# Kernel optimization log

Measured on AMD Instinct MI355X. Metric: run time of the kernel, lower is better.

Reference implementation:

```python
import jax, jax.numpy as jnp
import numpy as np

N_NODES = 50000
N_EDGES = 800000
IN_C, HID_C, OUT_C = 256, 256, 128


def setup_inputs() -> dict:
    key = jax.random.key(0)
    k1, k2, k3, k4 = jax.random.split(key, 4)
    x = jax.random.normal(k1, (N_NODES, IN_C), dtype=jnp.float32)
    edge_index = jax.random.randint(k2, (2, N_EDGES), 0, N_NODES, dtype=jnp.int64)
    W1 = jax.random.normal(k3, (IN_C, HID_C), dtype=jnp.float32) / np.sqrt(IN_C)
    b1 = jnp.zeros((HID_C,), dtype=jnp.float32)
    W2 = jax.random.normal(k4, (HID_C, OUT_C), dtype=jnp.float32) / np.sqrt(HID_C)
    b2 = jnp.zeros((OUT_C,), dtype=jnp.float32)
    return {"x": x, "edge_index": edge_index, "W1": W1, "b1": b1, "W2": W2, "b2": b2}


def _gcn_norm(edge_index, n_nodes):
    # Add self-loops, compute symmetric normalization D^-1/2 (A+I) D^-1/2 (PyG GCNConv default).
    loop = jnp.arange(n_nodes, dtype=edge_index.dtype)
    src = jnp.concatenate([edge_index[0], loop])  # [E+N]
    dst = jnp.concatenate([edge_index[1], loop])  # [E+N]
    deg = jax.ops.segment_sum(jnp.ones_like(dst, dtype=jnp.float32), dst, num_segments=n_nodes)
    dinv = jnp.where(deg > 0, 1.0 / jnp.sqrt(deg), 0.0)
    norm = dinv[src] * dinv[dst]  # [E+N]
    return src, dst, norm


def _gcn_conv(x, src, dst, norm, W, b, n_nodes):
    h = x @ W                                  # [N, out] dense GEMM first (PyG order)
    msg = h[src] * norm[:, None]               # gather + scale: [E+N, out]
    out = jax.ops.segment_sum(msg, dst, num_segments=n_nodes)  # scatter-add
    return out + b


def reference(x, edge_index, W1, b1, W2, b2):
    n = x.shape[0]
    src, dst, norm = _gcn_norm(edge_index, n)
    h = _gcn_conv(x, src, dst, norm, W1, b1, n)
    h = jax.nn.relu(h)
    # dropout is identity in eval mode
    return _gcn_conv(h, src, dst, norm, W2, b2, n)
```

## Files before the change

kernel.cpp:

```cpp
#include <hip/hip_runtime.h>
#include <cstdint>
#include <cstddef>


static constexpr int CH1 = 256;
static constexpr int CH2 = 128;

typedef __attribute__((ext_vector_type(8))) short bf16x8;
typedef __attribute__((ext_vector_type(4))) float f32x4;
typedef __attribute__((ext_vector_type(4))) unsigned short u16x4;

__device__ inline unsigned short f2bf(float f) {
  unsigned u = __builtin_bit_cast(unsigned, f);
  return (unsigned short)((u + 0x7fffu + ((u >> 16) & 1u)) >> 16);
}
__device__ inline float bf2f(unsigned short h) {
  return __builtin_bit_cast(float, (unsigned)h << 16);
}
__device__ inline float lo16(unsigned u) { return __builtin_bit_cast(float, u << 16); }
__device__ inline float hi16(unsigned u) { return __builtin_bit_cast(float, u & 0xffff0000u); }

__device__ inline void gload16(const void* g, void* l) {
  __builtin_amdgcn_global_load_lds(
      (const __attribute__((address_space(1))) unsigned int*)g,
      (__attribute__((address_space(3))) unsigned int*)l, 16, 0, 0);
}


__global__ void k_set_int(int* p, int v) { *p = v; }

__global__ void k_zero_int(int* __restrict__ p, int n) {
  int i = blockIdx.x * blockDim.x + threadIdx.x;
  if (i < n) p[i] = 0;
}

__global__ void k_detect_i32(const unsigned int* __restrict__ w, int nwords,
                             int* __restrict__ flag) {
  int i = blockIdx.x * blockDim.x + threadIdx.x;
  if (i < nwords && (i & 1) && w[i] != 0u) *flag = 1;
}

__global__ void k_cvt_deg(const void* __restrict__ raw, int* __restrict__ e32,
                          int* __restrict__ deg, int E, const int* __restrict__ flag) {
  int i = blockIdx.x * blockDim.x + threadIdx.x;
  if (i >= 2 * E) return;
  int v = (*flag) ? ((const int*)raw)[i] : (int)((const long long*)raw)[i];
  e32[i] = v;
  if (i >= E) atomicAdd(&deg[v], 1);
}

__global__ __launch_bounds__(256) void k_chunk_sum(const int* __restrict__ deg,
                                                   int* __restrict__ bsum, int N) {
  __shared__ int sh[256];
  int i = blockIdx.x * 256 + threadIdx.x;
  sh[threadIdx.x] = (i < N) ? deg[i] : 0;
  __syncthreads();
  for (int off = 128; off > 0; off >>= 1) {
    if (threadIdx.x < (unsigned)off) sh[threadIdx.x] += sh[threadIdx.x + off];
    __syncthreads();
  }
  if (threadIdx.x == 0) bsum[blockIdx.x] = sh[0];
}

__global__ __launch_bounds__(256) void k_scan_bsums(int* __restrict__ bsum, int nb) {
  __shared__ int sh[256];
  int t = threadIdx.x;
  int v = (t < nb) ? bsum[t] : 0;
  sh[t] = v;
  __syncthreads();
  for (int off = 1; off < 256; off <<= 1) {
    int add = (t >= off) ? sh[t - off] : 0;
    __syncthreads();
    sh[t] += add;
    __syncthreads();
  }
  if (t < nb) bsum[t] = sh[t] - v;
}

__global__ __launch_bounds__(256) void k_chunk_scan(
    const int* __restrict__ deg, const int* __restrict__ bsum,
    int* __restrict__ rowstart, int* __restrict__ cursor,
    float* __restrict__ dinv, int N, int E) {
  __shared__ int sh[256];
  int t = threadIdx.x;
  int i = blockIdx.x * 256 + t;
  int d = (i < N) ? deg[i] : 0;
  sh[t] = d;
  __syncthreads();
  for (int off = 1; off < 256; off <<= 1) {
    int add = (t >= off) ? sh[t - off] : 0;
    __syncthreads();
    sh[t] += add;
    __syncthreads();
  }
  if (i < N) {
    int rs = bsum[blockIdx.x] + sh[t] - d;
    rowstart[i] = rs;
    cursor[i]   = rs;
    dinv[i] = rsqrtf((float)(d + 1));
  }
  if (i == 0) rowstart[N] = E;
}

__global__ void k_fill(const int* __restrict__ src, const int* __restrict__ dst,
                       int* __restrict__ cursor, int* __restrict__ csr, int E) {
  int e = blockIdx.x * blockDim.x + threadIdx.x;
  if (e < E) {
    int pos = atomicAdd(&cursor[dst[e]], 1);
    csr[pos] = src[e];
  }
}


__global__ void k_split4(const float4* __restrict__ in, u16x4* __restrict__ oh,
                         u16x4* __restrict__ ol, int n4) {
  int i = blockIdx.x * blockDim.x + threadIdx.x;
  if (i >= n4) return;
  float4 v = in[i];
  u16x4 h, l;
  h.x = f2bf(v.x); l.x = f2bf(v.x - bf2f(h.x));
  h.y = f2bf(v.y); l.y = f2bf(v.y - bf2f(h.y));
  h.z = f2bf(v.z); l.z = f2bf(v.z - bf2f(h.z));
  h.w = f2bf(v.w); l.w = f2bf(v.w - bf2f(h.w));
  oh[i] = h; ol[i] = l;
}

__global__ void k_splitT(const float* __restrict__ W, unsigned short* __restrict__ oh,
                         unsigned short* __restrict__ ol, int K, int N) {
  int idx = blockIdx.x * blockDim.x + threadIdx.x;
  if (idx >= K * N) return;
  int k = idx / N, n = idx - k * N;
  float v = W[idx];
  unsigned short h = f2bf(v);
  oh[(size_t)n * K + k] = h;
  ol[(size_t)n * K + k] = f2bf(v - bf2f(h));
}

template <int BN>
__global__ __launch_bounds__(256) void k_gemm_mfma(
    const unsigned short* __restrict__ Ah, const unsigned short* __restrict__ Al,
    const unsigned short* __restrict__ Bh, const unsigned short* __restrict__ Bl,
    unsigned short* __restrict__ Co, int M, int K) {
  constexpr int BM = 64, BK = 32;
  constexpr int NF = BN / 64;
  constexpr int ASZ = BM * BK;
  constexpr int BSZ = BN * BK;
  __shared__ unsigned short lds[2][2 * ASZ + 2 * BSZ];
  const int t = threadIdx.x;
  const int w = t >> 6, l = t & 63;
  const int m0 = blockIdx.x * BM;
  const int lr = l & 15, lk = l >> 4;

  auto stage = [&](int buf, int k0) {
    unsigned short* base = lds[buf];
    {
      int row = t >> 2, p = t & 3;
      int s = p ^ ((row >> 1) & 3);
      int gm = m0 + row; if (gm >= M) gm = M - 1;
      size_t go = (size_t)gm * K + k0 + s * 8;
      gload16(Ah + go, base + (size_t)row * BK + p * 8);
      gload16(Al + go, base + ASZ + (size_t)row * BK + p * 8);
    }
    for (int i = t; i < BN * 4; i += 256) {
      int n = i >> 2, p = i & 3;
      int s = p ^ ((n >> 1) & 3);
      size_t go = (size_t)n * K + k0 + s * 8;
      gload16(Bh + go, base + 2 * ASZ + (size_t)n * BK + p * 8);
      gload16(Bl + go, base + 2 * ASZ + BSZ + (size_t)n * BK + p * 8);
    }
  };

  f32x4 acc[4][NF];
#pragma unroll
  for (int a = 0; a < 4; ++a)
#pragma unroll
    for (int b = 0; b < NF; ++b) acc[a][b] = (f32x4){0.f, 0.f, 0.f, 0.f};

  stage(0, 0);
  __syncthreads();
  const int nsteps = K / BK;
  for (int ks = 0; ks < nsteps; ++ks) {
    int cur = ks & 1;
    if (ks + 1 < nsteps) stage(cur ^ 1, (ks + 1) * BK);
    const unsigned short* base = lds[cur];
    bf16x8 ah[4], al[4], bh[NF], bl[NF];
#pragma unroll
    for (int fm = 0; fm < 4; ++fm) {
      int row = fm * 16 + lr;
      int p = lk ^ ((row >> 1) & 3);
      const unsigned short* a = base + row * BK + p * 8;
      ah[fm] = *(const bf16x8*)a;
      al[fm] = *(const bf16x8*)(a + ASZ);
    }
#pragma unroll
    for (int fb = 0; fb < NF; ++fb) {
      int n = w * (BN / 4) + fb * 16 + lr;
      int p = lk ^ ((n >> 1) & 3);
      const unsigned short* b = base + 2 * ASZ + n * BK + p * 8;
      bh[fb] = *(const bf16x8*)b;
      bl[fb] = *(const bf16x8*)(b + BSZ);
    }
#pragma unroll
    for (int fm = 0; fm < 4; ++fm)
#pragma unroll
      for (int fb = 0; fb < NF; ++fb) {
        acc[fm][fb] = __builtin_amdgcn_mfma_f32_16x16x32_bf16(ah[fm], bh[fb], acc[fm][fb], 0, 0, 0);
        acc[fm][fb] = __builtin_amdgcn_mfma_f32_16x16x32_bf16(ah[fm], bl[fb], acc[fm][fb], 0, 0, 0);
        acc[fm][fb] = __builtin_amdgcn_mfma_f32_16x16x32_bf16(al[fm], bh[fb], acc[fm][fb], 0, 0, 0);
      }
    __syncthreads();
  }
#pragma unroll
  for (int fm = 0; fm < 4; ++fm)
#pragma unroll
    for (int r = 0; r < 4; ++r) {
      int row = m0 + fm * 16 + lk * 4 + r;
      if (row < M) {
#pragma unroll
        for (int fb = 0; fb < NF; ++fb) {
          int col = w * (BN / 4) + fb * 16 + lr;
          Co[(size_t)row * BN + col] = f2bf(acc[fm][fb][r]);
        }
      }
    }
}

template <int C, int MODE>
__global__ __launch_bounds__(256) void k_agg_bf(
    const int* __restrict__ rowstart, const int* __restrict__ csr,
    const float* __restrict__ dinv, const unsigned short* __restrict__ h,
    const float* __restrict__ bias, float* __restrict__ out,
    unsigned short* __restrict__ oh, unsigned short* __restrict__ ol, int N) {
  constexpr int V = C / 64;
  static_assert(V == 2 || V == 4, "");
  int wv = blockIdx.x * 4 + (threadIdx.x >> 6);
  if (wv >= N) return;
  int lane = threadIdx.x & 63;
  int beg = rowstart[wv], end = rowstart[wv + 1];
  float acc[V] = {};
  int j = beg;
  if constexpr (V == 4) {
    const unsigned c8 = lane * 4;
    for (; j + 4 <= end; j += 4) {
      int s0 = csr[j], s1 = csr[j + 1], s2 = csr[j + 2], s3 = csr[j + 3];
      float w0 = dinv[s0], w1 = dinv[s1], w2 = dinv[s2], w3 = dinv[s3];
      uint2 a0 = *(const uint2*)(h + (size_t)s0 * C + c8);
      uint2 a1 = *(const uint2*)(h + (size_t)s1 * C + c8);
      uint2 a2 = *(const uint2*)(h + (size_t)s2 * C + c8);
      uint2 a3 = *(const uint2*)(h + (size_t)s3 * C + c8);
      acc[0] += w0 * lo16(a0.x) + w1 * lo16(a1.x) + w2 * lo16(a2.x) + w3 * lo16(a3.x);
      acc[1] += w0 * hi16(a0.x) + w1 * hi16(a1.x) + w2 * hi16(a2.x) + w3 * hi16(a3.x);
      acc[2] += w0 * lo16(a0.y) + w1 * lo16(a1.y) + w2 * lo16(a2.y) + w3 * lo16(a3.y);
      acc[3] += w0 * hi16(a0.y) + w1 * hi16(a1.y) + w2 * hi16(a2.y) + w3 * hi16(a3.y);
    }
    for (; j < end; ++j) {
      int s = csr[j];
      float ws = dinv[s];
      uint2 a = *(const uint2*)(h + (size_t)s * C + c8);
      acc[0] += ws * lo16(a.x); acc[1] += ws * hi16(a.x);
      acc[2] += ws * lo16(a.y); acc[3] += ws * hi16(a.y);
    }
    float dv = dinv[wv], sw = dv * dv;
    uint2 hh = *(const uint2*)(h + (size_t)wv * C + c8);
    float4 bb = *(const float4*)(bias + lane * 4);
    float o0 = dv * acc[0] + sw * lo16(hh.x) + bb.x;
    float o1 = dv * acc[1] + sw * hi16(hh.x) + bb.y;
    float o2 = dv * acc[2] + sw * lo16(hh.y) + bb.z;
    float o3 = dv * acc[3] + sw * hi16(hh.y) + bb.w;
    if constexpr (MODE == 1) {
      o0 = fmaxf(o0, 0.f); o1 = fmaxf(o1, 0.f);
      o2 = fmaxf(o2, 0.f); o3 = fmaxf(o3, 0.f);
      u16x4 vh, vl;
      vh.x = f2bf(o0); vl.x = f2bf(o0 - bf2f(vh.x));
      vh.y = f2bf(o1); vl.y = f2bf(o1 - bf2f(vh.y));
      vh.z = f2bf(o2); vl.z = f2bf(o2 - bf2f(vh.z));
      vh.w = f2bf(o3); vl.w = f2bf(o3 - bf2f(vh.w));
      *(u16x4*)(oh + (size_t)wv * C + c8) = vh;
      *(u16x4*)(ol + (size_t)wv * C + c8) = vl;
    } else {
      *(float4*)(out + (size_t)wv * C + lane * 4) = make_float4(o0, o1, o2, o3);
    }
  } else {
    const unsigned c4 = lane * 2;
    for (; j + 4 <= end; j += 4) {
      int s0 = csr[j], s1 = csr[j + 1], s2 = csr[j + 2], s3 = csr[j + 3];
      float w0 = dinv[s0], w1 = dinv[s1], w2 = dinv[s2], w3 = dinv[s3];
      unsigned a0 = *(const unsigned*)(h + (size_t)s0 * C + c4);
      unsigned a1 = *(const unsigned*)(h + (size_t)s1 * C + c4);
      unsigned a2 = *(const unsigned*)(h + (size_t)s2 * C + c4);
      unsigned a3 = *(const unsigned*)(h + (size_t)s3 * C + c4);
      acc[0] += w0 * lo16(a0) + w1 * lo16(a1) + w2 * lo16(a2) + w3 * lo16(a3);
      acc[1] += w0 * hi16(a0) + w1 * hi16(a1) + w2 * hi16(a2) + w3 * hi16(a3);
    }
    for (; j < end; ++j) {
      int s = csr[j];
      float ws = dinv[s];
      unsigned a = *(const unsigned*)(h + (size_t)s * C + c4);
      acc[0] += ws * lo16(a); acc[1] += ws * hi16(a);
    }
    float dv = dinv[wv], sw = dv * dv;
    unsigned hh = *(const unsigned*)(h + (size_t)wv * C + c4);
    float2 bb = *(const float2*)(bias + lane * 2);
    float o0 = dv * acc[0] + sw * lo16(hh) + bb.x;
    float o1 = dv * acc[1] + sw * hi16(hh) + bb.y;
    *(float2*)(out + (size_t)wv * C + lane * 2) = make_float2(o0, o1);
  }
}


extern "C" void kernel_launch(void* const* d_in, const int* in_sizes, int n_in,
                              void* d_out, int out_size, void* d_ws, size_t ws_size,
                              hipStream_t stream) {
  const float* x  = (const float*)d_in[0];
  const void*  ei = d_in[1];
  const float* W1 = (const float*)d_in[2];
  const float* b1 = (const float*)d_in[3];
  const float* W2 = (const float*)d_in[4];
  const float* b2 = (const float*)d_in[5];
  float* out = (float*)d_out;

  const int N = in_sizes[0] / CH1;
  const int E = in_sizes[1] / 2;

  char* w = (char*)d_ws;
  size_t off = 0;
  auto alloc = [&](size_t bytes) -> void* {
    void* p = w + off;
    off += (bytes + 255) & ~(size_t)255;
    return p;
  };
  int*   deg      = (int*)alloc((size_t)N * 4);
  int*   flag     = (int*)alloc(256);
  int*   e32      = (int*)alloc((size_t)2 * E * 4);
  int*   rowstart = (int*)alloc((size_t)(N + 1) * 4);
  int*   cursor   = (int*)alloc((size_t)N * 4);
  int*   bsum     = (int*)alloc(256 * 4);
  int*   csr      = (int*)alloc((size_t)E * 4);
  float* dinv     = (float*)alloc((size_t)N * 4);
  unsigned short* xh  = (unsigned short*)alloc((size_t)N * CH1 * 2);
  unsigned short* xl  = (unsigned short*)alloc((size_t)N * CH1 * 2);
  unsigned short* h1  = (unsigned short*)alloc((size_t)N * CH1 * 2);
  unsigned short* h2  = (unsigned short*)alloc((size_t)N * CH2 * 2);
  unsigned short* w1th = (unsigned short*)alloc((size_t)CH1 * CH1 * 2);
  unsigned short* w1tl = (unsigned short*)alloc((size_t)CH1 * CH1 * 2);
  unsigned short* w2th = (unsigned short*)alloc((size_t)CH1 * CH2 * 2);
  unsigned short* w2tl = (unsigned short*)alloc((size_t)CH1 * CH2 * 2);

  const int* srcI = e32;
  const int* dstI = e32 + E;

  dim3 blk(256);
  auto cdiv = [](long long a, long long b) { return (int)((a + b - 1) / b); };
  const int nchunks = cdiv(N, 256);

  k_set_int<<<1, 1, 0, stream>>>(flag, 0);
  k_detect_i32<<<cdiv(2LL * E, 256), blk, 0, stream>>>((const unsigned int*)ei, 2 * E, flag);
  k_zero_int<<<cdiv(N, 256), blk, 0, stream>>>(deg, N);
  k_cvt_deg<<<cdiv(2LL * E, 256), blk, 0, stream>>>(ei, e32, deg, E, flag);
  k_chunk_sum<<<nchunks, blk, 0, stream>>>(deg, bsum, N);
  k_scan_bsums<<<1, blk, 0, stream>>>(bsum, nchunks);
  k_chunk_scan<<<nchunks, blk, 0, stream>>>(deg, bsum, rowstart, cursor, dinv, N, E);
  k_fill<<<cdiv(E, 256), blk, 0, stream>>>(srcI, dstI, cursor, csr, E);

  k_split4<<<cdiv((long long)N * CH1 / 4, 256), blk, 0, stream>>>(
      (const float4*)x, (u16x4*)xh, (u16x4*)xl, N * CH1 / 4);
  k_splitT<<<cdiv(CH1 * CH1, 256), blk, 0, stream>>>(W1, w1th, w1tl, CH1, CH1);
  k_splitT<<<cdiv(CH1 * CH2, 256), blk, 0, stream>>>(W2, w2th, w2tl, CH1, CH2);

  k_gemm_mfma<CH1><<<cdiv(N, 64), blk, 0, stream>>>(xh, xl, w1th, w1tl, h1, N, CH1);
  k_agg_bf<CH1, 1><<<cdiv(N, 4), blk, 0, stream>>>(rowstart, csr, dinv, h1, b1,
                                                   nullptr, xh, xl, N);
  k_gemm_mfma<CH2><<<cdiv(N, 64), blk, 0, stream>>>(xh, xl, w2th, w2tl, h2, N, CH1);
  k_agg_bf<CH2, 0><<<cdiv(N, 4), blk, 0, stream>>>(rowstart, csr, dinv, h2, b2,
                                                   out, nullptr, nullptr, N);
}
```

Baseline: 278.1 us.

## Pre-scale GEMM output by source dinv and widen aggregation gathers to 16B

The GEMM epilogue now multiplies each output row by dinv[row], so the aggregation no longer gathers dinv per neighbor and the self-loop term folds into the plain sum. The aggregation kernel is restructured so each node is handled by a sub-group of lanes (32 or 16) that each load 8 bf16 channels with a 16-byte load, packing two or four nodes per wave. This removes the random dinv gathers and gives wider memory transactions, with fewer lanes working per edge list. Two tiny init kernels are also merged into one launch.

```diff
diff --git a/kernel.cpp b/kernel.cpp
--- a/kernel.cpp
+++ b/kernel.cpp
@@ -27,11 +27,10 @@
 }
 
 
-__global__ void k_set_int(int* p, int v) { *p = v; }
-
-__global__ void k_zero_int(int* __restrict__ p, int n) {
+__global__ void k_init_deg(int* __restrict__ deg, int n, int* __restrict__ flag) {
   int i = blockIdx.x * blockDim.x + threadIdx.x;
-  if (i < n) p[i] = 0;
+  if (i < n) deg[i] = 0;
+  if (i == 0) *flag = 0;
 }
 
 __global__ void k_detect_i32(const unsigned int* __restrict__ w, int nwords,
@@ -140,7 +139,7 @@
 __global__ __launch_bounds__(256) void k_gemm_mfma(
     const unsigned short* __restrict__ Ah, const unsigned short* __restrict__ Al,
     const unsigned short* __restrict__ Bh, const unsigned short* __restrict__ Bl,
-    unsigned short* __restrict__ Co, int M, int K) {
+    const float* __restrict__ dinv, unsigned short* __restrict__ Co, int M, int K) {
   constexpr int BM = 64, BK = 32;
   constexpr int NF = BN / 64;
   constexpr int ASZ = BM * BK;
@@ -216,94 +215,85 @@
     for (int r = 0; r < 4; ++r) {
       int row = m0 + fm * 16 + lk * 4 + r;
       if (row < M) {
+        float dv = dinv[row];
 #pragma unroll
         for (int fb = 0; fb < NF; ++fb) {
           int col = w * (BN / 4) + fb * 16 + lr;
-          Co[(size_t)row * BN + col] = f2bf(acc[fm][fb][r]);
+          Co[(size_t)row * BN + col] = f2bf(dv * acc[fm][fb][r]);
         }
       }
     }
 }
 
-template <int C, int MODE>
-__global__ __launch_bounds__(256) void k_agg_bf(
+template <int C, int GL, int MODE>
+__global__ __launch_bounds__(256) void k_agg(
     const int* __restrict__ rowstart, const int* __restrict__ csr,
-    const float* __restrict__ dinv, const unsigned short* __restrict__ h,
+    const float* __restrict__ dinv, const unsigned short* __restrict__ g,
     const float* __restrict__ bias, float* __restrict__ out,
     unsigned short* __restrict__ oh, unsigned short* __restrict__ ol, int N) {
-  constexpr int V = C / 64;
-  static_assert(V == 2 || V == 4, "");
-  int wv = blockIdx.x * 4 + (threadIdx.x >> 6);
-  if (wv >= N) return;
+  constexpr int GPW = 64 / GL;
+  static_assert(C / GL == 8, "8 bf16 channels per lane");
+  int wave = (blockIdx.x * 256 + threadIdx.x) >> 6;
   int lane = threadIdx.x & 63;
-  int beg = rowstart[wv], end = rowstart[wv + 1];
-  float acc[V] = {};
+  int v = wave * GPW + lane / GL;
+  if (v >= N) return;
+  const int c0 = (lane % GL) * 8;
+  const unsigned short* __restrict__ gc = g + c0;
+
+  float a0 = 0.f, a1 = 0.f, a2 = 0.f, a3 = 0.f;
+  float a4 = 0.f, a5 = 0.f, a6 = 0.f, a7 = 0.f;
+#define ACC8(u)                                          \
+  a0 += lo16((u).x); a1 += hi16((u).x);                  \
+  a2 += lo16((u).y); a3 += hi16((u).y);                  \
+  a4 += lo16((u).z); a5 += hi16((u).z);                  \
+  a6 += lo16((u).w); a7 += hi16((u).w);
+
+  int beg = rowstart[v], end = rowstart[v + 1];
   int j = beg;
-  if constexpr (V == 4) {
-    const unsigned c8 = lane * 4;
-    for (; j + 4 <= end; j += 4) {
-      int s0 = csr[j], s1 = csr[j + 1], s2 = csr[j + 2], s3 = csr[j + 3];
-      float w0 = dinv[s0], w1 = dinv[s1], w2 = dinv[s2], w3 = dinv[s3];
-      uint2 a0 = *(const uint2*)(h + (size_t)s0 * C + c8);
-      uint2 a1 = *(const uint2*)(h + (size_t)s1 * C + c8);
-      uint2 a2 = *(const uint2*)(h + (size_t)s2 * C + c8);
-      uint2 a3 = *(const uint2*)(h + (size_t)s3 * C + c8);
-      acc[0] += w0 * lo16(a0.x) + w1 * lo16(a1.x) + w2 * lo16(a2.x) + w3 * lo16(a3.x);
-      acc[1] += w0 * hi16(a0.x) + w1 * hi16(a1.x) + w2 * hi16(a2.x) + w3 * hi16(a3.x);
-      acc[2] += w0 * lo16(a0.y) + w1 * lo16(a1.y) + w2 * lo16(a2.y) + w3 * lo16(a3.y);
-      acc[3] += w0 * hi16(a0.y) + w1 * hi16(a1.y) + w2 * hi16(a2.y) + w3 * hi16(a3.y);
-    }
-    for (; j < end; ++j) {
-      int s = csr[j];
-      float ws = dinv[s];
-      uint2 a = *(const uint2*)(h + (size_t)s * C + c8);
-      acc[0] += ws * lo16(a.x); acc[1] += ws * hi16(a.x);
-      acc[2] += ws * lo16(a.y); acc[3] += ws * hi16(a.y);
-    }
-    float dv = dinv[wv], sw = dv * dv;
-    uint2 hh = *(const uint2*)(h + (size_t)wv * C + c8);
-    float4 bb = *(const float4*)(bias + lane * 4);
-    float o0 = dv * acc[0] + sw * lo16(hh.x) + bb.x;
-    float o1 = dv * acc[1] + sw * hi16(hh.x) + bb.y;
-    float o2 = dv * acc[2] + sw * lo16(hh.y) + bb.z;
-    float o3 = dv * acc[3] + sw * hi16(hh.y) + bb.w;
-    if constexpr (MODE == 1) {
-      o0 = fmaxf(o0, 0.f); o1 = fmaxf(o1, 0.f);
-      o2 = fmaxf(o2, 0.f); o3 = fmaxf(o3, 0.f);
-      u16x4 vh, vl;
-      vh.x = f2bf(o0); vl.x = f2bf(o0 - bf2f(vh.x));
-      vh.y = f2bf(o1); vl.y = f2bf(o1 - bf2f(vh.y));
-      vh.z = f2bf(o2); vl.z = f2bf(o2 - bf2f(vh.z));
-      vh.w = f2bf(o3); vl.w = f2bf(o3 - bf2f(vh.w));
-      *(u16x4*)(oh + (size_t)wv * C + c8) = vh;
-      *(u16x4*)(ol + (size_t)wv * C + c8) = vl;
-    } else {
-      *(float4*)(out + (size_t)wv * C + lane * 4) = make_float4(o0, o1, o2, o3);
-    }
+  for (; j + 4 <= end; j += 4) {
+    int s0 = csr[j], s1 = csr[j + 1], s2 = csr[j + 2], s3 = csr[j + 3];
+    uint4 r0 = *(const uint4*)(gc + (size_t)s0 * C);
+    uint4 r1 = *(const uint4*)(gc + (size_t)s1 * C);
+    uint4 r2 = *(const uint4*)(gc + (size_t)s2 * C);
+    uint4 r3 = *(const uint4*)(gc + (size_t)s3 * C);
+    ACC8(r0) ACC8(r1) ACC8(r2) ACC8(r3)
+  }
+  for (; j < end; ++j) {
+    uint4 r = *(const uint4*)(gc + (size_t)csr[j] * C);
+    ACC8(r)
+  }
+  {
+    uint4 r = *(const uint4*)(gc + (size_t)v * C);
+    ACC8(r)
+  }
+#undef ACC8
+
+  float dv = dinv[v];
+  float4 bA = *(const float4*)(bias + c0);
+  float4 bB = *(const float4*)(bias + c0 + 4);
+  float o0 = dv * a0 + bA.x, o1 = dv * a1 + bA.y;
+  float o2 = dv * a2 + bA.z, o3 = dv * a3 + bA.w;
+  float o4 = dv * a4 + bB.x, o5 = dv * a5 + bB.y;
+  float o6 = dv * a6 + bB.z, o7 = dv * a7 + bB.w;
+  if constexpr (MODE == 1) {
+    o0 = fmaxf(o0, 0.f); o1 = fmaxf(o1, 0.f); o2 = fmaxf(o2, 0.f); o3 = fmaxf(o3, 0.f);
+    o4 = fmaxf(o4, 0.f); o5 = fmaxf(o5, 0.f); o6 = fmaxf(o6, 0.f); o7 = fmaxf(o7, 0.f);
+    u16x4 vh, vl;
+    vh.x = f2bf(o0); vl.x = f2bf(o0 - bf2f(vh.x));
+    vh.y = f2bf(o1); vl.y = f2bf(o1 - bf2f(vh.y));
+    vh.z = f2bf(o2); vl.z = f2bf(o2 - bf2f(vh.z));
+    vh.w = f2bf(o3); vl.w = f2bf(o3 - bf2f(vh.w));
+    *(u16x4*)(oh + (size_t)v * C + c0) = vh;
+    *(u16x4*)(ol + (size_t)v * C + c0) = vl;
+    vh.x = f2bf(o4); vl.x = f2bf(o4 - bf2f(vh.x));
+    vh.y = f2bf(o5); vl.y = f2bf(o5 - bf2f(vh.y));
+    vh.z = f2bf(o6); vl.z = f2bf(o6 - bf2f(vh.z));
+    vh.w = f2bf(o7); vl.w = f2bf(o7 - bf2f(vh.w));
+    *(u16x4*)(oh + (size_t)v * C + c0 + 4) = vh;
+    *(u16x4*)(ol + (size_t)v * C + c0 + 4) = vl;
   } else {
-    const unsigned c4 = lane * 2;
-    for (; j + 4 <= end; j += 4) {
-      int s0 = csr[j], s1 = csr[j + 1], s2 = csr[j + 2], s3 = csr[j + 3];
-      float w0 = dinv[s0], w1 = dinv[s1], w2 = dinv[s2], w3 = dinv[s3];
-      unsigned a0 = *(const unsigned*)(h + (size_t)s0 * C + c4);
-      unsigned a1 = *(const unsigned*)(h + (size_t)s1 * C + c4);
-      unsigned a2 = *(const unsigned*)(h + (size_t)s2 * C + c4);
-      unsigned a3 = *(const unsigned*)(h + (size_t)s3 * C + c4);
-      acc[0] += w0 * lo16(a0) + w1 * lo16(a1) + w2 * lo16(a2) + w3 * lo16(a3);
-      acc[1] += w0 * hi16(a0) + w1 * hi16(a1) + w2 * hi16(a2) + w3 * hi16(a3);
-    }
-    for (; j < end; ++j) {
-      int s = csr[j];
-      float ws = dinv[s];
-      unsigned a = *(const unsigned*)(h + (size_t)s * C + c4);
-      acc[0] += ws * lo16(a); acc[1] += ws * hi16(a);
-    }
-    float dv = dinv[wv], sw = dv * dv;
-    unsigned hh = *(const unsigned*)(h + (size_t)wv * C + c4);
-    float2 bb = *(const float2*)(bias + lane * 2);
-    float o0 = dv * acc[0] + sw * lo16(hh) + bb.x;
-    float o1 = dv * acc[1] + sw * hi16(hh) + bb.y;
-    *(float2*)(out + (size_t)wv * C + lane * 2) = make_float2(o0, o1);
+    *(float4*)(out + (size_t)v * C + c0) = make_float4(o0, o1, o2, o3);
+    *(float4*)(out + (size_t)v * C + c0 + 4) = make_float4(o4, o5, o6, o7);
   }
 }
 
@@ -339,8 +329,8 @@
   float* dinv     = (float*)alloc((size_t)N * 4);
   unsigned short* xh  = (unsigned short*)alloc((size_t)N * CH1 * 2);
   unsigned short* xl  = (unsigned short*)alloc((size_t)N * CH1 * 2);
-  unsigned short* h1  = (unsigned short*)alloc((size_t)N * CH1 * 2);
-  unsigned short* h2  = (unsigned short*)alloc((size_t)N * CH2 * 2);
+  unsigned short* g1  = (unsigned short*)alloc((size_t)N * CH1 * 2);
+  unsigned short* g2  = (unsigned short*)alloc((size_t)N * CH2 * 2);
   unsigned short* w1th = (unsigned short*)alloc((size_t)CH1 * CH1 * 2);
   unsigned short* w1tl = (unsigned short*)alloc((size_t)CH1 * CH1 * 2);
   unsigned short* w2th = (unsigned short*)alloc((size_t)CH1 * CH2 * 2);
@@ -353,9 +343,8 @@
   auto cdiv = [](long long a, long long b) { return (int)((a + b - 1) / b); };
   const int nchunks = cdiv(N, 256);
 
-  k_set_int<<<1, 1, 0, stream>>>(flag, 0);
+  k_init_deg<<<cdiv(N, 256), blk, 0, stream>>>(deg, N, flag);
   k_detect_i32<<<cdiv(2LL * E, 256), blk, 0, stream>>>((const unsigned int*)ei, 2 * E, flag);
-  k_zero_int<<<cdiv(N, 256), blk, 0, stream>>>(deg, N);
   k_cvt_deg<<<cdiv(2LL * E, 256), blk, 0, stream>>>(ei, e32, deg, E, flag);
   k_chunk_sum<<<nchunks, blk, 0, stream>>>(deg, bsum, N);
   k_scan_bsums<<<1, blk, 0, stream>>>(bsum, nchunks);
@@ -367,10 +356,11 @@
   k_splitT<<<cdiv(CH1 * CH1, 256), blk, 0, stream>>>(W1, w1th, w1tl, CH1, CH1);
   k_splitT<<<cdiv(CH1 * CH2, 256), blk, 0, stream>>>(W2, w2th, w2tl, CH1, CH2);
 
-  k_gemm_mfma<CH1><<<cdiv(N, 64), blk, 0, stream>>>(xh, xl, w1th, w1tl, h1, N, CH1);
-  k_agg_bf<CH1, 1><<<cdiv(N, 4), blk, 0, stream>>>(rowstart, csr, dinv, h1, b1,
-                                                   nullptr, xh, xl, N);
-  k_gemm_mfma<CH2><<<cdiv(N, 64), blk, 0, stream>>>(xh, xl, w2th, w2tl, h2, N, CH1);
-  k_agg_bf<CH2, 0><<<cdiv(N, 4), blk, 0, stream>>>(rowstart, csr, dinv, h2, b2,
-                                                   out, nullptr, nullptr, N);
-}
+  k_gemm_mfma<CH1><<<cdiv(N, 64), blk, 0, stream>>>(xh, xl, w1th, w1tl, dinv, g1, N, CH1);
+  k_agg<CH1, 32, 1><<<cdiv((long long)N * 32, 256), blk, 0, stream>>>(
+      rowstart, csr, dinv, g1, b1, nullptr, xh, xl, N);
+
+  k_gemm_mfma<CH2><<<cdiv(N, 64), blk, 0, stream>>>(xh, xl, w2th, w2tl, dinv, g2, N, CH1);
+  k_agg<CH2, 16, 0><<<cdiv((long long)N * 16, 256), blk, 0, stream>>>(
+      rowstart, csr, dinv, g2, b2, out, nullptr, nullptr, N);
+}
```

After: 282.7 us. Within noise of the previous version (+1.7%).
